# Performance work log

Measured on AMD Instinct MI355X. Metric: run time of the kernel, lower is better.

Reference implementation:

```python
import jax, jax.numpy as jnp
import numpy as np

B, S, D, H = 4, 1024, 1024, 16
DK = D // H  # d_k = 64

def setup_inputs() -> dict:
    key = jax.random.key(0)
    ks = jax.random.split(key, 6)
    sc = 0.02
    return {
        "x": jax.random.normal(ks[0], (B, S, D), jnp.float32),
        "bias": jax.random.normal(ks[1], (H, S, S), jnp.float32),
        "Wq": jax.random.normal(ks[2], (D, D), jnp.float32) * sc,
        "Wk": jax.random.normal(ks[3], (D, D), jnp.float32) * sc,
        "Wv": jax.random.normal(ks[4], (D, D), jnp.float32) * sc,
        "Wo": jax.random.normal(ks[5], (D, D), jnp.float32) * sc,
    }

def _split_heads(t):
    # [B,S,D] -> [B,H,S,DK]
    b, s, _ = t.shape
    return t.reshape(b, s, H, DK).transpose(0, 2, 1, 3)

def reference(x, bias, Wq, Wk, Wv, Wo):
    q = _split_heads(x @ Wq)
    k = _split_heads(x @ Wk)
    v = _split_heads(x @ Wv)
    scale = jnp.asarray(DK, x.dtype) ** 0.5
    # [B,H,S,S] scores with additive per-head bias (broadcast over batch)
    attn = jnp.einsum('bhqd,bhkd->bhqk', q / scale, k) + bias[None]
    attn = jax.nn.softmax(attn, axis=-1)
    ctx = jnp.einsum('bhqk,bhkd->bhqd', attn, v)
    ctx = ctx.transpose(0, 2, 1, 3).reshape(x.shape[0], x.shape[1], -1)
    out = ctx @ Wo
    return (out, attn)
```

## Files before the change

kernel.cpp:

```cpp
#include <hip/hip_runtime.h>
#include <hip/hip_bf16.h>


typedef __bf16 bf16_t;
typedef __bf16 bf16x4 __attribute__((ext_vector_type(4)));
typedef __bf16 bf16x8 __attribute__((ext_vector_type(8)));
typedef float f32x4 __attribute__((ext_vector_type(4)));

#define MFMA16(a, b, c) __builtin_amdgcn_mfma_f32_16x16x32_bf16(a, b, c, 0, 0, 0)

__global__ __launch_bounds__(256) void cast_f32_bf16(const float* __restrict__ in,
                                                     bf16_t* __restrict__ out, int n4) {
    int i = blockIdx.x * blockDim.x + threadIdx.x;
    if (i >= n4) return;
    float4 v = reinterpret_cast<const float4*>(in)[i];
    bf16x4 o = { (bf16_t)v.x, (bf16_t)v.y, (bf16_t)v.z, (bf16_t)v.w };
    reinterpret_cast<bf16x4*>(out)[i] = o;
}

__global__ __launch_bounds__(1024) void transpose_cast_w(const float* __restrict__ w0,
                                                         const float* __restrict__ w1,
                                                         const float* __restrict__ w2,
                                                         const float* __restrict__ w3,
                                                         bf16_t* __restrict__ wt) {
    __shared__ float tile[32][33];
    const float* src = (blockIdx.z == 0) ? w0 : (blockIdx.z == 1) ? w1
                     : (blockIdx.z == 2) ? w2 : w3;
    bf16_t* dst = wt + (size_t)blockIdx.z * 1024 * 1024;
    int r0 = blockIdx.y * 32, c0 = blockIdx.x * 32;
    tile[threadIdx.y][threadIdx.x] = src[(size_t)(r0 + threadIdx.y) * 1024 + c0 + threadIdx.x];
    __syncthreads();
    dst[(size_t)(c0 + threadIdx.y) * 1024 + r0 + threadIdx.x] = (bf16_t)tile[threadIdx.x][threadIdx.y];
}

#define GEMM_BODY(A, BT)                                                                 \
    __shared__ bf16_t As[128 * 32];                                                      \
    __shared__ bf16_t Bs[128 * 32];                                                      \
    const int tid = threadIdx.x;                                                         \
    const int lane = tid & 63, wave = tid >> 6;                                          \
    const int lr = lane & 15, lg = lane >> 4;                                            \
    const int m_base = blockIdx.x * 128, n_base = blockIdx.y * 128;                      \
    const int wm = (wave >> 1) * 64, wn = (wave & 1) * 64;                               \
    const int srow = tid >> 1;                                                           \
    const int sl0 = (tid & 1) * 2;                                                       \
    const int sl1 = sl0 + 1;                                                             \
    const int off0 = srow * 32 + ((sl0 ^ ((srow >> 1) & 3)) * 8);                        \
    const int off1 = srow * 32 + ((sl1 ^ ((srow >> 1) & 3)) * 8);                        \
    const bf16_t* aptr = (A) + (size_t)(m_base + srow) * 1024 + sl0 * 8;                 \
    const bf16_t* bptr = (BT) + (size_t)(n_base + srow) * 1024 + sl0 * 8;                \
    bf16x8 ra0 = *reinterpret_cast<const bf16x8*>(aptr);                                 \
    bf16x8 ra1 = *reinterpret_cast<const bf16x8*>(aptr + 8);                             \
    bf16x8 rb0 = *reinterpret_cast<const bf16x8*>(bptr);                                 \
    bf16x8 rb1 = *reinterpret_cast<const bf16x8*>(bptr + 8);                             \
    f32x4 acc[4][4] = {};                                                                \
    for (int kb = 32; kb <= 1024; kb += 32) {                                            \
        __syncthreads();                                                                 \
        *reinterpret_cast<bf16x8*>(&As[off0]) = ra0;                                     \
        *reinterpret_cast<bf16x8*>(&As[off1]) = ra1;                                     \
        *reinterpret_cast<bf16x8*>(&Bs[off0]) = rb0;                                     \
        *reinterpret_cast<bf16x8*>(&Bs[off1]) = rb1;                                     \
        if (kb < 1024) {                                                                 \
            ra0 = *reinterpret_cast<const bf16x8*>(aptr + kb);                           \
            ra1 = *reinterpret_cast<const bf16x8*>(aptr + kb + 8);                       \
            rb0 = *reinterpret_cast<const bf16x8*>(bptr + kb);                           \
            rb1 = *reinterpret_cast<const bf16x8*>(bptr + kb + 8);                       \
        }                                                                                \
        __syncthreads();                                                                 \
        bf16x8 af[4], bfr[4];                                                            \
        _Pragma("unroll") for (int i = 0; i < 4; ++i) {                                  \
            const int row = wm + i * 16 + lr;                                            \
            af[i] = *reinterpret_cast<const bf16x8*>(                                    \
                &As[row * 32 + ((lg ^ ((row >> 1) & 3)) * 8)]);                          \
        }                                                                                \
        _Pragma("unroll") for (int j = 0; j < 4; ++j) {                                  \
            const int row = wn + j * 16 + lr;                                            \
            bfr[j] = *reinterpret_cast<const bf16x8*>(                                   \
                &Bs[row * 32 + ((lg ^ ((row >> 1) & 3)) * 8)]);                          \
        }                                                                                \
        _Pragma("unroll") for (int i = 0; i < 4; ++i)                                    \
            _Pragma("unroll") for (int j = 0; j < 4; ++j)                                \
                acc[i][j] = MFMA16(af[i], bfr[j], acc[i][j]);                            \
    }

__global__ __launch_bounds__(256, 3) void gemm_qkv(const bf16_t* __restrict__ A,
                                                   const bf16_t* __restrict__ wT,
                                                   bf16_t* __restrict__ qhp,
                                                   bf16_t* __restrict__ khp,
                                                   bf16_t* __restrict__ vp) {
    const int z = blockIdx.z;
    const bf16_t* BT = wT + ((size_t)z << 20);
    GEMM_BODY(A, BT)
    bf16_t* dst = (z == 0) ? qhp : (z == 1) ? khp : vp;
    const float scale = (z == 0) ? 0.125f : 1.0f;
#pragma unroll
    for (int i = 0; i < 4; ++i)
#pragma unroll
        for (int j = 0; j < 4; ++j)
#pragma unroll
            for (int r = 0; r < 4; ++r) {
                const int row = m_base + wm + i * 16 + lg * 4 + r;
                const int col = n_base + wn + j * 16 + lr;
                const float v = acc[i][j][r] * scale;
                const int b = row >> 10, s = row & 1023;
                const int h = col >> 6, d = col & 63;
                const size_t bh16 = (size_t)(b * 16 + h) << 16;
                if (z == 2)
                    dst[bh16 + ((s >> 5) << 11) + d * 32 + (s & 31)] = (bf16_t)v;
                else
                    dst[bh16 + ((d >> 5) << 15) + s * 32 + (d & 31)] = (bf16_t)v;
            }
}

__global__ __launch_bounds__(256, 3) void gemm_out(const bf16_t* __restrict__ A,
                                                   const bf16_t* __restrict__ BT,
                                                   float* __restrict__ out) {
    GEMM_BODY(A, BT)
#pragma unroll
    for (int i = 0; i < 4; ++i)
#pragma unroll
        for (int j = 0; j < 4; ++j)
#pragma unroll
            for (int r = 0; r < 4; ++r) {
                const int row = m_base + wm + i * 16 + lg * 4 + r;
                const int col = n_base + wn + j * 16 + lr;
                out[(size_t)row * 1024 + col] = acc[i][j][r];
            }
}

__global__ __launch_bounds__(256, 2) void fused_attn(const bf16_t* __restrict__ qhp,
                                                     const bf16_t* __restrict__ khp,
                                                     const bf16_t* __restrict__ vp,
                                                     const float* __restrict__ bias,
                                                     float* __restrict__ attn,
                                                     bf16_t* __restrict__ ctxb) {
    __shared__ f32x4 wlds4[4][1024];
    __shared__ float smaxp[128];
    __shared__ float ssump[128];
    const int lane = threadIdx.x & 63;
    const int wave = threadIdx.x >> 6;
    const int lr = lane & 15, lg = lane >> 4;

    const int g = blockIdx.x;
    const int j = g >> 3;
    const int h = (g & 7) + 8 * (j >> 7);
    const int qt = (j >> 2) & 31;
    const int b = j & 3;
    const int bh = b * 16 + h;
    const int m0 = qt * 32;

    const bf16_t* qbase = qhp + ((size_t)bh << 16);
    const bf16x8 aqA0 = *reinterpret_cast<const bf16x8*>(qbase + (m0 + lr) * 32 + lg * 8);
    const bf16x8 aqA1 = *reinterpret_cast<const bf16x8*>(qbase + 32768 + (m0 + lr) * 32 + lg * 8);
    const bf16x8 aqB0 = *reinterpret_cast<const bf16x8*>(qbase + (m0 + 16 + lr) * 32 + lg * 8);
    const bf16x8 aqB1 = *reinterpret_cast<const bf16x8*>(qbase + 32768 + (m0 + 16 + lr) * 32 + lg * 8);

    const int c0 = wave * 256;
    const bf16_t* kp0 = khp + ((size_t)bh << 16) + (size_t)(c0 + lr) * 32 + lg * 8;

    char* tw = reinterpret_cast<char*>(&wlds4[wave][0]);
    const int myswz = (lr & 7) << 4;

    const float* bb0 = bias + ((size_t)h << 20) + (size_t)m0 * 1024 + c0;
#pragma unroll
    for (int i = 0; i < 16; ++i) {
        const int co = (lane * 4) ^ ((i & 7) * 4);
        f32x4 bv = *reinterpret_cast<const f32x4*>(bb0 + (size_t)i * 1024 + co);
        *reinterpret_cast<f32x4*>(tw + i * 1024 + lane * 16) = bv;
    }
    f32x4 acc0[16];
#pragma unroll
    for (int f = 0; f < 16; ++f)
        acc0[f] = *reinterpret_cast<const f32x4*>(tw + lr * 1024 + ((f * 64 + lg * 16) ^ myswz));

    const float* bb1 = bb0 + 16 * 1024;
#pragma unroll
    for (int i = 0; i < 16; ++i) {
        const int co = (lane * 4) ^ ((i & 7) * 4);
        f32x4 bv = *reinterpret_cast<const f32x4*>(bb1 + (size_t)i * 1024 + co);
        *reinterpret_cast<f32x4*>(tw + i * 1024 + lane * 16) = bv;
    }
    f32x4 acc1[16];
#pragma unroll
    for (int f = 0; f < 16; ++f)
        acc1[f] = *reinterpret_cast<const f32x4*>(tw + lr * 1024 + ((f * 64 + lg * 16) ^ myswz));

#pragma unroll
    for (int half = 0; half < 2; ++half) {
        const bf16x8 aqA = half ? aqA1 : aqA0;
        const bf16x8 aqB = half ? aqB1 : aqB0;
#pragma unroll
        for (int bt = 0; bt < 2; ++bt) {
            bf16x8 kf[8];
#pragma unroll
            for (int u = 0; u < 8; ++u)
                kf[u] = *reinterpret_cast<const bf16x8*>(
                    kp0 + half * 32768 + (bt * 8 + u) * 512);
#pragma unroll
            for (int u = 0; u < 8; ++u) {
                acc0[bt * 8 + u] = MFMA16(kf[u], aqA, acc0[bt * 8 + u]);
                acc1[bt * 8 + u] = MFMA16(kf[u], aqB, acc1[bt * 8 + u]);
            }
        }
    }

    f32x4 m40 = acc0[0], m41 = acc1[0];
#pragma unroll
    for (int f = 1; f < 16; ++f) {
#pragma unroll
        for (int r = 0; r < 4; ++r) {
            m40[r] = fmaxf(m40[r], acc0[f][r]);
            m41[r] = fmaxf(m41[r], acc1[f][r]);
        }
    }
    float mx0 = fmaxf(fmaxf(m40[0], m40[1]), fmaxf(m40[2], m40[3]));
    float mx1 = fmaxf(fmaxf(m41[0], m41[1]), fmaxf(m41[2], m41[3]));
    mx0 = fmaxf(mx0, __shfl_xor(mx0, 16));
    mx0 = fmaxf(mx0, __shfl_xor(mx0, 32));
    mx1 = fmaxf(mx1, __shfl_xor(mx1, 16));
    mx1 = fmaxf(mx1, __shfl_xor(mx1, 32));
    if (lane < 16) {
        smaxp[wave * 16 + lr] = mx0;
        smaxp[64 + wave * 16 + lr] = mx1;
    }
    __syncthreads();
    const float gm0 = fmaxf(fmaxf(smaxp[lr], smaxp[16 + lr]),
                            fmaxf(smaxp[32 + lr], smaxp[48 + lr]));
    const float gm1 = fmaxf(fmaxf(smaxp[64 + lr], smaxp[80 + lr]),
                            fmaxf(smaxp[96 + lr], smaxp[112 + lr]));

    f32x4 s40 = {0.f, 0.f, 0.f, 0.f}, s41 = {0.f, 0.f, 0.f, 0.f};
#pragma unroll
    for (int f = 0; f < 16; ++f) {
#pragma unroll
        for (int r = 0; r < 4; ++r) {
            const float e0 = __expf(acc0[f][r] - gm0);
            const float e1 = __expf(acc1[f][r] - gm1);
            acc0[f][r] = e0;
            acc1[f][r] = e1;
            s40[r] += e0;
            s41[r] += e1;
        }
    }
    float sm0 = (s40[0] + s40[1]) + (s40[2] + s40[3]);
    float sm1 = (s41[0] + s41[1]) + (s41[2] + s41[3]);
    sm0 += __shfl_xor(sm0, 16);
    sm0 += __shfl_xor(sm0, 32);
    sm1 += __shfl_xor(sm1, 16);
    sm1 += __shfl_xor(sm1, 32);
    if (lane < 16) {
        ssump[wave * 16 + lr] = sm0;
        ssump[64 + wave * 16 + lr] = sm1;
    }
    __syncthreads();
    const float invl0 = 1.0f / (ssump[lr] + ssump[16 + lr] + ssump[32 + lr] + ssump[48 + lr]);
    const float invl1 = 1.0f / (ssump[64 + lr] + ssump[80 + lr] + ssump[96 + lr] + ssump[112 + lr]);

    const bf16_t* vpb = vp + ((size_t)bh << 16) + (size_t)(wave * 8) * 2048 + lr * 32 + lg * 8;
    bf16x8 vf0[4][4];
#pragma unroll
    for (int ks = 0; ks < 4; ++ks)
#pragma unroll
        for (int f2 = 0; f2 < 4; ++f2)
            vf0[ks][f2] = *reinterpret_cast<const bf16x8*>(vpb + ks * 2048 + f2 * 512);

#pragma unroll
    for (int f = 0; f < 16; ++f) {
        f32x4 v0 = acc0[f], v1 = acc1[f];
#pragma unroll
        for (int r = 0; r < 4; ++r) { v0[r] *= invl0; v1[r] *= invl1; }
        bf16x4 p0 = { (bf16_t)v0[0], (bf16_t)v0[1], (bf16_t)v0[2], (bf16_t)v0[3] };
        bf16x4 p1 = { (bf16_t)v1[0], (bf16_t)v1[1], (bf16_t)v1[2], (bf16_t)v1[3] };
        const int ro = lr * 512 + ((f * 32 + lg * 8) ^ myswz);
        *reinterpret_cast<bf16x4*>(tw + ro) = p0;
        *reinterpret_cast<bf16x4*>(tw + 8192 + ro) = p1;
    }

    {
        float* obase = attn + ((size_t)bh << 20) + (size_t)m0 * 1024 + c0;
#pragma unroll
        for (int i = 0; i < 16; ++i) {
            const int cc = (lane * 4) ^ ((i & 7) * 8);
            bf16x4 q0 = *reinterpret_cast<const bf16x4*>(tw + i * 512 + lane * 8);
            bf16x4 q1 = *reinterpret_cast<const bf16x4*>(tw + 8192 + i * 512 + lane * 8);
            f32x4 w0 = { (float)q0[0], (float)q0[1], (float)q0[2], (float)q0[3] };
            f32x4 w1 = { (float)q1[0], (float)q1[1], (float)q1[2], (float)q1[3] };
            *reinterpret_cast<f32x4*>(obase + (size_t)i * 1024 + cc) = w0;
            *reinterpret_cast<f32x4*>(obase + (size_t)(16 + i) * 1024 + cc) = w1;
        }
    }

    f32x4 cacc0[4], cacc1[4];
#pragma unroll
    for (int f2 = 0; f2 < 4; ++f2) {
        cacc0[f2] = (f32x4){0.f, 0.f, 0.f, 0.f};
        cacc1[f2] = (f32x4){0.f, 0.f, 0.f, 0.f};
    }
    bf16x8 vf1[4][4];
#pragma unroll
    for (int ks = 0; ks < 4; ++ks)
#pragma unroll
        for (int f2 = 0; f2 < 4; ++f2)
            vf1[ks][f2] = *reinterpret_cast<const bf16x8*>(vpb + (4 + ks) * 2048 + f2 * 512);

#pragma unroll
    for (int ks = 0; ks < 4; ++ks) {
        const int po = lr * 512 + ((ks * 64 + lg * 16) ^ myswz);
        bf16x8 pa0 = *reinterpret_cast<const bf16x8*>(tw + po);
        bf16x8 pa1 = *reinterpret_cast<const bf16x8*>(tw + 8192 + po);
#pragma unroll
        for (int f2 = 0; f2 < 4; ++f2) {
            cacc0[f2] = MFMA16(pa0, vf0[ks][f2], cacc0[f2]);
            cacc1[f2] = MFMA16(pa1, vf0[ks][f2], cacc1[f2]);
        }
    }
#pragma unroll
    for (int ks = 4; ks < 8; ++ks) {
        const int po = lr * 512 + ((ks * 64 + lg * 16) ^ myswz);
        bf16x8 pa0 = *reinterpret_cast<const bf16x8*>(tw + po);
        bf16x8 pa1 = *reinterpret_cast<const bf16x8*>(tw + 8192 + po);
#pragma unroll
        for (int f2 = 0; f2 < 4; ++f2) {
            cacc0[f2] = MFMA16(pa0, vf1[ks - 4][f2], cacc0[f2]);
            cacc1[f2] = MFMA16(pa1, vf1[ks - 4][f2], cacc1[f2]);
        }
    }

    {
        float* credw = reinterpret_cast<float*>(tw);
#pragma unroll
        for (int f2 = 0; f2 < 4; ++f2)
#pragma unroll
            for (int r = 0; r < 4; ++r) {
                credw[(lg * 4 + r) * 64 + f2 * 16 + lr] = cacc0[f2][r];
                credw[1024 + (lg * 4 + r) * 64 + f2 * 16 + lr] = cacc1[f2][r];
            }
    }
    __syncthreads();
    const int row_l = wave * 4 + lg;
    const int dk0 = lr * 4;
#pragma unroll
    for (int t = 0; t < 2; ++t) {
        f32x4 s0 = *reinterpret_cast<const f32x4*>(
            reinterpret_cast<const float*>(&wlds4[0][0]) + t * 1024 + row_l * 64 + dk0);
        f32x4 s1 = *reinterpret_cast<const f32x4*>(
            reinterpret_cast<const float*>(&wlds4[1][0]) + t * 1024 + row_l * 64 + dk0);
        f32x4 s2 = *reinterpret_cast<const f32x4*>(
            reinterpret_cast<const float*>(&wlds4[2][0]) + t * 1024 + row_l * 64 + dk0);
        f32x4 s3 = *reinterpret_cast<const f32x4*>(
            reinterpret_cast<const float*>(&wlds4[3][0]) + t * 1024 + row_l * 64 + dk0);
        f32x4 st = (s0 + s1) + (s2 + s3);
        bf16x4 o4 = { (bf16_t)st[0], (bf16_t)st[1], (bf16_t)st[2], (bf16_t)st[3] };
        *reinterpret_cast<bf16x4*>(
            &ctxb[(size_t)(b * 1024 + m0 + t * 16 + row_l) * 1024 + h * 64 + dk0]) = o4;
    }
}

extern "C" void kernel_launch(void* const* d_in, const int* in_sizes, int n_in,
                              void* d_out, int out_size, void* d_ws, size_t ws_size,
                              hipStream_t stream) {
    const float* x    = (const float*)d_in[0];
    const float* bias = (const float*)d_in[1];
    const float* Wq   = (const float*)d_in[2];
    const float* Wk   = (const float*)d_in[3];
    const float* Wv   = (const float*)d_in[4];
    const float* Wo   = (const float*)d_in[5];
    float* out  = (float*)d_out;
    float* attn = out + (size_t)4 * 1024 * 1024;

    char* ws = (char*)d_ws;
    bf16_t* xb   = (bf16_t*)(ws);
    bf16_t* wT   = (bf16_t*)(ws + ((size_t)8 << 20));
    bf16_t* qhp  = (bf16_t*)(ws + ((size_t)16 << 20));
    bf16_t* khp  = (bf16_t*)(ws + ((size_t)24 << 20));
    bf16_t* vp   = (bf16_t*)(ws + ((size_t)32 << 20));
    bf16_t* ctxb = (bf16_t*)(ws + ((size_t)40 << 20));
    bf16_t* woT = wT + ((size_t)3 << 20);

    cast_f32_bf16<<<dim3(4096), dim3(256), 0, stream>>>(x, xb, 1024 * 1024);
    transpose_cast_w<<<dim3(32, 32, 4), dim3(32, 32), 0, stream>>>(Wq, Wk, Wv, Wo, wT);

    gemm_qkv<<<dim3(32, 8, 3), dim3(256), 0, stream>>>(xb, wT, qhp, khp, vp);

    fused_attn<<<dim3(2048), dim3(256), 0, stream>>>(qhp, khp, vp, bias, attn, ctxb);

    gemm_out<<<dim3(32, 8), dim3(256), 0, stream>>>(ctxb, woT, out);
}
```

Measured before the change: 180.8 us.

## Double-buffer GEMM LDS tiles with direct global-to-LDS async loads

The shared GEMM body now copies A and B tiles straight from global memory into LDS with global_load_lds, instead of staging them through registers. The LDS buffers are doubled so the next k-tile is fetched while the current one feeds the MFMAs. This leaves one barrier per iteration instead of two and frees the staging registers. In exchange it doubles LDS use per block, which may lower occupancy. Correctness depends on the barrier waiting for the async LDS writes to finish.

```diff
diff --git a/kernel.cpp b/kernel.cpp
--- a/kernel.cpp
+++ b/kernel.cpp
@@ -8,6 +8,11 @@
 typedef float f32x4 __attribute__((ext_vector_type(4)));
 
 #define MFMA16(a, b, c) __builtin_amdgcn_mfma_f32_16x16x32_bf16(a, b, c, 0, 0, 0)
+
+#define GLOAD16(g, l)                                                        \
+    __builtin_amdgcn_global_load_lds(                                        \
+        (const __attribute__((address_space(1))) unsigned int*)(g),          \
+        (__attribute__((address_space(3))) unsigned int*)(l), 16, 0, 0)
 
 __global__ __launch_bounds__(256) void cast_f32_bf16(const float* __restrict__ in,
                                                      bf16_t* __restrict__ out, int n4) {
@@ -34,52 +39,52 @@
 }
 
 #define GEMM_BODY(A, BT)                                                                 \
-    __shared__ bf16_t As[128 * 32];                                                      \
-    __shared__ bf16_t Bs[128 * 32];                                                      \
+    __shared__ bf16_t As[2][128 * 32];                                                   \
+    __shared__ bf16_t Bs[2][128 * 32];                                                   \
     const int tid = threadIdx.x;                                                         \
     const int lane = tid & 63, wave = tid >> 6;                                          \
     const int lr = lane & 15, lg = lane >> 4;                                            \
     const int m_base = blockIdx.x * 128, n_base = blockIdx.y * 128;                      \
     const int wm = (wave >> 1) * 64, wn = (wave & 1) * 64;                               \
-    const int srow = tid >> 1;                                                           \
-    const int sl0 = (tid & 1) * 2;                                                       \
-    const int sl1 = sl0 + 1;                                                             \
-    const int off0 = srow * 32 + ((sl0 ^ ((srow >> 1) & 3)) * 8);                        \
-    const int off1 = srow * 32 + ((sl1 ^ ((srow >> 1) & 3)) * 8);                        \
-    const bf16_t* aptr = (A) + (size_t)(m_base + srow) * 1024 + sl0 * 8;                 \
-    const bf16_t* bptr = (BT) + (size_t)(n_base + srow) * 1024 + sl0 * 8;                \
-    bf16x8 ra0 = *reinterpret_cast<const bf16x8*>(aptr);                                 \
-    bf16x8 ra1 = *reinterpret_cast<const bf16x8*>(aptr + 8);                             \
-    bf16x8 rb0 = *reinterpret_cast<const bf16x8*>(bptr);                                 \
-    bf16x8 rb1 = *reinterpret_cast<const bf16x8*>(bptr + 8);                             \
+    const int c0_ = wave, c1_ = wave + 4;                                                \
+    const int r0_ = c0_ * 16 + (lane >> 2);                                              \
+    const int r1_ = c1_ * 16 + (lane >> 2);                                              \
+    const int s0_ = (lane & 3) ^ ((r0_ >> 1) & 3);                                       \
+    const int s1_ = (lane & 3) ^ ((r1_ >> 1) & 3);                                       \
+    const bf16_t* ga0_ = (A) + (size_t)(m_base + r0_) * 1024 + s0_ * 8;                  \
+    const bf16_t* ga1_ = (A) + (size_t)(m_base + r1_) * 1024 + s1_ * 8;                  \
+    const bf16_t* gb0_ = (BT) + (size_t)(n_base + r0_) * 1024 + s0_ * 8;                 \
+    const bf16_t* gb1_ = (BT) + (size_t)(n_base + r1_) * 1024 + s1_ * 8;                 \
     f32x4 acc[4][4] = {};                                                                \
-    for (int kb = 32; kb <= 1024; kb += 32) {                                            \
-        __syncthreads();                                                                 \
-        *reinterpret_cast<bf16x8*>(&As[off0]) = ra0;                                     \
-        *reinterpret_cast<bf16x8*>(&As[off1]) = ra1;                                     \
-        *reinterpret_cast<bf16x8*>(&Bs[off0]) = rb0;                                     \
-        *reinterpret_cast<bf16x8*>(&Bs[off1]) = rb1;                                     \
-        if (kb < 1024) {                                                                 \
-            ra0 = *reinterpret_cast<const bf16x8*>(aptr + kb);                           \
-            ra1 = *reinterpret_cast<const bf16x8*>(aptr + kb + 8);                       \
-            rb0 = *reinterpret_cast<const bf16x8*>(bptr + kb);                           \
-            rb1 = *reinterpret_cast<const bf16x8*>(bptr + kb + 8);                       \
+    GLOAD16(ga0_, &As[0][c0_ * 512]);                                                    \
+    GLOAD16(ga1_, &As[0][c1_ * 512]);                                                    \
+    GLOAD16(gb0_, &Bs[0][c0_ * 512]);                                                    \
+    GLOAD16(gb1_, &Bs[0][c1_ * 512]);                                                    \
+    int cur_ = 0;                                                                        \
+    for (int t = 0; t < 32; ++t) {                                                       \
+        __syncthreads();                           \
+        if (t < 31) {                                                                    \
+            const int kb = (t + 1) * 32;                                                 \
+            GLOAD16(ga0_ + kb, &As[cur_ ^ 1][c0_ * 512]);                                \
+            GLOAD16(ga1_ + kb, &As[cur_ ^ 1][c1_ * 512]);                                \
+            GLOAD16(gb0_ + kb, &Bs[cur_ ^ 1][c0_ * 512]);                                \
+            GLOAD16(gb1_ + kb, &Bs[cur_ ^ 1][c1_ * 512]);                                \
         }                                                                                \
-        __syncthreads();                                                                 \
         bf16x8 af[4], bfr[4];                                                            \
         _Pragma("unroll") for (int i = 0; i < 4; ++i) {                                  \
             const int row = wm + i * 16 + lr;                                            \
             af[i] = *reinterpret_cast<const bf16x8*>(                                    \
-                &As[row * 32 + ((lg ^ ((row >> 1) & 3)) * 8)]);                          \
+                &As[cur_][row * 32 + ((lg ^ ((row >> 1) & 3)) * 8)]);                    \
         }                                                                                \
         _Pragma("unroll") for (int j = 0; j < 4; ++j) {                                  \
             const int row = wn + j * 16 + lr;                                            \
             bfr[j] = *reinterpret_cast<const bf16x8*>(                                   \
-                &Bs[row * 32 + ((lg ^ ((row >> 1) & 3)) * 8)]);                          \
+                &Bs[cur_][row * 32 + ((lg ^ ((row >> 1) & 3)) * 8)]);                    \
         }                                                                                \
         _Pragma("unroll") for (int i = 0; i < 4; ++i)                                    \
             _Pragma("unroll") for (int j = 0; j < 4; ++j)                                \
                 acc[i][j] = MFMA16(af[i], bfr[j], acc[i][j]);                            \
+        cur_ ^= 1;                                                                       \
     }
 
 __global__ __launch_bounds__(256, 3) void gemm_qkv(const bf16_t* __restrict__ A,
```

New measurement: 183.4 us. Within noise of the previous version (+1.4%).
